# Kernel optimization log

Hardware: AMD Instinct MI355X
Metric: run time of the kernel (lower is better)

## Reference

```python
import jax, jax.numpy as jnp
import numpy as np
import math

HEADS = 8
DIM_HEAD = 64


def setup_inputs() -> dict:
    key = jax.random.key(0)
    k1, k2, k3 = jax.random.split(key, 3)
    b, n, dim = 4, 2048, 512
    inner = HEADS * DIM_HEAD  # 512
    x = jax.random.normal(k1, (b, n, dim), dtype=jnp.float32)
    W_qkv = jax.random.normal(k2, (dim, 4 * inner), dtype=jnp.float32) * (dim ** -0.5)
    W_out = jax.random.normal(k3, (2 * inner, dim), dtype=jnp.float32) * ((2 * inner) ** -0.5)
    b_out = jnp.zeros((dim,), dtype=jnp.float32)
    return {"x": x, "W_qkv": W_qkv, "W_out": W_out, "b_out": b_out}


def reference(x, W_qkv, W_out, b_out):
    b, n, d = x.shape
    h, dh = HEADS, DIM_HEAD
    scale = dh ** -0.5
    qkvt = x @ W_qkv  # [b, n, 4*h*dh]
    q, k, v, t = jnp.split(qkvt, 4, axis=-1)
    # 'b n (h d) -> b h n d'
    def to_heads(z):
        return z.reshape(b, n, h, dh).transpose(0, 2, 1, 3)
    q, k, v, t = map(to_heads, (q, k, v, t))

    # Branch 1: standard softmax attention
    dots = jnp.einsum('bhid,bhjd->bhij', q, k) * scale
    attn1 = jax.nn.softmax(dots, axis=-1)
    out1 = jnp.einsum('bhij,bhjd->bhid', attn1, v)

    # Branch 2: fixed positional-decay attention (shared across b, h; no repeat needed)
    pos = jnp.arange(1, n + 1, dtype=x.dtype)  # linspace(1, n, n)
    tg = jnp.abs(pos[None, :] - pos[:, None])  # |j - i|, [n, n]
    attn2 = jnp.exp(-tg / jnp.asarray(math.e, dtype=x.dtype))
    # NOTE: original divides by sum(-1) WITHOUT keepdim -> broadcasts over columns:
    # attn2[i, j] / sum_k attn2[j, k]
    attn2 = attn2 / attn2.sum(-1)
    out2 = jnp.einsum('ij,bhjd->bhid', attn2, t)

    out = jnp.concatenate([out1, out2], axis=-1)  # [b, h, n, 2*dh]
    out = out.transpose(0, 2, 1, 3).reshape(b, n, 2 * h * dh)  # 'b h n d -> b n (h d)'
    return out @ W_out + b_out
```

## Files before the change

kernel.cpp:

```cpp
#include <hip/hip_runtime.h>
#include <hip/hip_bf16.h>

#define B_ 4
#define N_ 2048
#define D_ 512
#define H_ 8
#define DH_ 64

typedef float float4_ __attribute__((ext_vector_type(4)));
typedef int int2_ __attribute__((ext_vector_type(2)));
typedef int int4_ __attribute__((ext_vector_type(4)));
typedef unsigned short ushort4_ __attribute__((ext_vector_type(4)));
typedef unsigned short ushort8_ __attribute__((ext_vector_type(8)));
typedef __bf16 bf16x8 __attribute__((ext_vector_type(8)));
typedef _Float16 half2_ __attribute__((ext_vector_type(2)));
typedef _Float16 half4_ __attribute__((ext_vector_type(4)));
typedef _Float16 half8_ __attribute__((ext_vector_type(8)));

#if __has_builtin(__builtin_amdgcn_exp2f)
#define EXP2(x) __builtin_amdgcn_exp2f(x)
#else
#define EXP2(x) exp2f(x)
#endif

__device__ __forceinline__ float b2f(unsigned short u) {
  union { unsigned int u; float f; } v; v.u = ((unsigned int)u) << 16; return v.f;
}
__device__ __forceinline__ unsigned short f2b(float f) {
  union { float f; unsigned int u; } v; v.f = f;
  unsigned int r = v.u + 0x7fffu + ((v.u >> 16) & 1u);
  return (unsigned short)(r >> 16);
}
__device__ __forceinline__ half4_ pk4(float a, float b, float c, float d) {
  half2_ lo = __builtin_bit_cast(half2_, __builtin_amdgcn_cvt_pkrtz(a, b));
  half2_ hi = __builtin_bit_cast(half2_, __builtin_amdgcn_cvt_pkrtz(c, d));
  return __builtin_bit_cast(half4_,
      (int2_){__builtin_bit_cast(int, lo), __builtin_bit_cast(int, hi)});
}

#define GLD16(gp, lp)                                                        \
  __builtin_amdgcn_global_load_lds(                                          \
      (const __attribute__((address_space(1))) unsigned int*)(gp),           \
      (__attribute__((address_space(3))) unsigned int*)(lp), 16, 0, 0)

__device__ __forceinline__ bool detect_fp32_local(
    const unsigned short* __restrict__ xhdr, int* cnt_sh) {
  if (threadIdx.x == 0) *cnt_sh = 0;
  __syncthreads();
  unsigned int e = (xhdr[threadIdx.x] >> 7) & 0xFFu;
  if (e >= 134u) atomicAdd(cnt_sh, 1);
  __syncthreads();
  return *cnt_sh > 16;
}

__device__ __forceinline__ void transpose_conv(
    const void* __restrict__ src, unsigned short* __restrict__ dst,
    int R, int C, int bx, int by, bool ofp) {
  __shared__ unsigned short tile[32][33];
  const int c0 = bx * 32, r0 = by * 32;
  const int tx = threadIdx.x & 31, ty = threadIdx.x >> 5;
#pragma unroll
  for (int k = 0; k < 4; ++k) {
    int r = ty + k * 8;
    long idx = (long)(r0 + r) * C + c0 + tx;
    tile[r][tx] = ofp ? f2b(((const float*)src)[idx])
                      : ((const unsigned short*)src)[idx];
  }
  __syncthreads();
#pragma unroll
  for (int k = 0; k < 4; ++k) {
    int c = ty + k * 8;
    dst[(long)(c0 + c) * R + r0 + tx] = tile[tx][c];
  }
}

__global__ __launch_bounds__(256) void prep_all(
    const void* __restrict__ xraw, const void* __restrict__ Wqraw,
    const void* __restrict__ Woraw, unsigned short* __restrict__ xb,
    unsigned short* __restrict__ WqT, unsigned short* __restrict__ WoT,
    unsigned short* __restrict__ Wband) {
  __shared__ int cnt_sh;
  const bool ofp = detect_fp32_local((const unsigned short*)xraw, &cnt_sh);
  const int bid = blockIdx.x;
  if (bid < 4096) {
    int i4 = bid * 256 + threadIdx.x;
    ushort4_ o;
    if (ofp) {
      float4_ v = ((const float4_*)xraw)[i4];
      o[0] = f2b(v[0]); o[1] = f2b(v[1]); o[2] = f2b(v[2]); o[3] = f2b(v[3]);
    } else {
      o = ((const ushort4_*)xraw)[i4];
    }
    *(ushort4_*)(xb + (long)i4 * 4) = o;
  } else if (bid < 5120) {
    const int b2 = bid - 4096;
    transpose_conv(Wqraw, WqT, 512, 2048, b2 % 64, b2 / 64, ofp);
  } else if (bid < 5632) {
    const int b2 = bid - 5120;
    transpose_conv(Woraw, WoT, 1024, 512, b2 % 16, b2 / 16, ofp);
  } else {
    constexpr float INV_E = 0.36787944117144233f;
    constexpr float R1 = 0.69220062755534635f;
    constexpr float INV_1MR = 3.2488706f;
    const int i = bid - 5632;
    const int krel = threadIdx.x;
    const int j = (i >> 6) * 64 - 96 + krel;
    float c = 0.f;
    if (j >= 0 && j < N_) {
      float wgt = __expf(-fabsf((float)(i - j)) * INV_E);
      float rj = __expf(-(float)j * INV_E);
      float rnj = __expf(-(float)(N_ - 1 - j) * INV_E);
      float S = 1.f + R1 * (2.f - rj - rnj) * INV_1MR;
      c = wgt / S;
    }
    _Float16 hv = (_Float16)c;
    Wband[i * 256 + krel] = __builtin_bit_cast(unsigned short, hv);
  }
}

#define MFMA16x32(d, a, b) \
  d = __builtin_amdgcn_mfma_f32_16x16x32_bf16(a, b, d, 0, 0, 0)

__global__ __launch_bounds__(512, 2) void gemm256(
    const unsigned short* __restrict__ A, const unsigned short* __restrict__ Bt,
    unsigned short* __restrict__ C, int M, int N, int K) {
  __shared__ unsigned short As[2][16384];
  __shared__ unsigned short Bs[2][16384];
  const int tid = threadIdx.x;
  const int w = tid >> 6, lane = tid & 63, l16 = lane & 15, quad = lane >> 4;
  const int wm = w >> 2, wn = w & 3;
  const long tm = (long)blockIdx.x * 256, tn = (long)blockIdx.y * 256;

  const int srow = tid >> 3;
  const int sch = (tid & 7) ^ (srow & 7);
  const unsigned short* gA = A + (tm + srow) * (long)K + sch * 8;
  const unsigned short* gB = Bt + (tn + srow) * (long)K + sch * 8;

  const int xr8 = l16 & 7;
  const int ch0 = ((0 + quad) ^ xr8) * 8;
  const int ch1 = ((4 + quad) ^ xr8) * 8;
  const int rowA0 = (wm * 128 + l16) * 64;
  const int rowB0 = (wn * 64 + l16) * 64;

  float4_ acc[8][4] = {};

  auto stage = [&](int t, int bufn) __attribute__((always_inline)) {
#pragma unroll
    for (int r = 0; r < 4; ++r)
      GLD16(gA + (long)(r * 64) * K + t * 64, &As[bufn][r * 4096 + w * 512]);
#pragma unroll
    for (int r = 0; r < 4; ++r)
      GLD16(gB + (long)(r * 64) * K + t * 64, &Bs[bufn][r * 4096 + w * 512]);
  };

  stage(0, 0);
  asm volatile("s_waitcnt vmcnt(0)" ::: "memory");
  __builtin_amdgcn_s_barrier();

  const int NT = K >> 6;
  for (int t = 0; t < NT; ++t) {
    const int buf = t & 1;
    const unsigned short* as = As[buf];
    const unsigned short* bs = Bs[buf];
    bf16x8 af[8], bq[4], br[4];
#pragma unroll
    for (int mi = 0; mi < 4; ++mi) {
      af[mi * 2]     = __builtin_bit_cast(bf16x8, *(const int4_*)&as[rowA0 + mi * 1024 + ch0]);
      af[mi * 2 + 1] = __builtin_bit_cast(bf16x8, *(const int4_*)&as[rowA0 + mi * 1024 + ch1]);
    }
#pragma unroll
    for (int ni = 0; ni < 2; ++ni) {
      bq[ni * 2]     = __builtin_bit_cast(bf16x8, *(const int4_*)&bs[rowB0 + ni * 1024 + ch0]);
      bq[ni * 2 + 1] = __builtin_bit_cast(bf16x8, *(const int4_*)&bs[rowB0 + ni * 1024 + ch1]);
    }
    if (t + 1 < NT) stage(t + 1, buf ^ 1);
    __builtin_amdgcn_s_barrier();
    asm volatile("s_waitcnt lgkmcnt(0)" ::: "memory");
    __builtin_amdgcn_sched_barrier(0);
    __builtin_amdgcn_s_setprio(1);
#pragma unroll
    for (int mi = 0; mi < 4; ++mi)
#pragma unroll
      for (int ni = 0; ni < 2; ++ni) {
        MFMA16x32(acc[mi][ni], af[mi * 2], bq[ni * 2]);
        MFMA16x32(acc[mi][ni], af[mi * 2 + 1], bq[ni * 2 + 1]);
      }
    __builtin_amdgcn_s_setprio(0);
    __builtin_amdgcn_s_barrier();
#pragma unroll
    for (int ni = 0; ni < 2; ++ni) {
      br[ni * 2]     = __builtin_bit_cast(bf16x8, *(const int4_*)&bs[rowB0 + (2 + ni) * 1024 + ch0]);
      br[ni * 2 + 1] = __builtin_bit_cast(bf16x8, *(const int4_*)&bs[rowB0 + (2 + ni) * 1024 + ch1]);
    }
    __builtin_amdgcn_s_barrier();
    asm volatile("s_waitcnt lgkmcnt(0)" ::: "memory");
    __builtin_amdgcn_sched_barrier(0);
    __builtin_amdgcn_s_setprio(1);
#pragma unroll
    for (int mi = 0; mi < 4; ++mi)
#pragma unroll
      for (int ni = 0; ni < 2; ++ni) {
        MFMA16x32(acc[mi][2 + ni], af[mi * 2], br[ni * 2]);
        MFMA16x32(acc[mi][2 + ni], af[mi * 2 + 1], br[ni * 2 + 1]);
      }
    __builtin_amdgcn_s_setprio(0);
    __builtin_amdgcn_s_barrier();
#pragma unroll
    for (int mi = 0; mi < 4; ++mi) {
      af[mi * 2]     = __builtin_bit_cast(bf16x8, *(const int4_*)&as[rowA0 + (4 + mi) * 1024 + ch0]);
      af[mi * 2 + 1] = __builtin_bit_cast(bf16x8, *(const int4_*)&as[rowA0 + (4 + mi) * 1024 + ch1]);
    }
    __builtin_amdgcn_s_barrier();
    asm volatile("s_waitcnt lgkmcnt(0)" ::: "memory");
    __builtin_amdgcn_sched_barrier(0);
    __builtin_amdgcn_s_setprio(1);
#pragma unroll
    for (int mi = 0; mi < 4; ++mi)
#pragma unroll
      for (int ni = 0; ni < 2; ++ni) {
        MFMA16x32(acc[4 + mi][2 + ni], af[mi * 2], br[ni * 2]);
        MFMA16x32(acc[4 + mi][2 + ni], af[mi * 2 + 1], br[ni * 2 + 1]);
      }
    __builtin_amdgcn_s_setprio(0);
    __builtin_amdgcn_s_barrier();
#pragma unroll
    for (int ni = 0; ni < 2; ++ni) {
      bq[ni * 2]     = __builtin_bit_cast(bf16x8, *(const int4_*)&bs[rowB0 + ni * 1024 + ch0]);
      bq[ni * 2 + 1] = __builtin_bit_cast(bf16x8, *(const int4_*)&bs[rowB0 + ni * 1024 + ch1]);
    }
    __builtin_amdgcn_s_barrier();
    asm volatile("s_waitcnt lgkmcnt(0)" ::: "memory");
    __builtin_amdgcn_sched_barrier(0);
    __builtin_amdgcn_s_setprio(1);
#pragma unroll
    for (int mi = 0; mi < 4; ++mi)
#pragma unroll
      for (int ni = 0; ni < 2; ++ni) {
        MFMA16x32(acc[4 + mi][ni], af[mi * 2], bq[ni * 2]);
        MFMA16x32(acc[4 + mi][ni], af[mi * 2 + 1], bq[ni * 2 + 1]);
      }
    __builtin_amdgcn_s_setprio(0);
    asm volatile("s_waitcnt vmcnt(0)" ::: "memory");
    __builtin_amdgcn_sched_barrier(0);
    __builtin_amdgcn_s_barrier();
  }
#pragma unroll
  for (int ni = 0; ni < 4; ++ni) {
    long col = tn + wn * 64 + ni * 16 + l16;
#pragma unroll
    for (int mi = 0; mi < 8; ++mi)
#pragma unroll
      for (int r = 0; r < 4; ++r) {
        long row = tm + wm * 128 + mi * 16 + quad * 4 + r;
        C[row * N + col] = f2b(acc[mi][ni][r]);
      }
  }
}

__global__ __launch_bounds__(256) void gemm_n64(
    const unsigned short* __restrict__ A, const unsigned short* __restrict__ Bt,
    void* __restrict__ C, const void* __restrict__ bias_raw,
    int M, int N, int K, const unsigned short* __restrict__ xhdr) {
  __shared__ int cnt_sh;
  const bool ofp = detect_fp32_local(xhdr, &cnt_sh);
  __shared__ unsigned short As[128 * 32];
  __shared__ unsigned short Bs[64 * 32];
  const int tid = threadIdx.x;
  const int w = tid >> 6, lane = tid & 63, l16 = lane & 15, quad = lane >> 4;
  const int wm = (w & 1) * 64, wn = (w >> 1) * 32;
  const long tm = (long)blockIdx.x * 128, tn = (long)blockIdx.y * 64;
  const int srowA = w * 32 + (lane >> 2);
  const int srowB = w * 16 + (lane >> 2);
  const int scol = (lane & 3) * 8;
  float4_ acc[4][2] = {};
  for (int k0 = 0; k0 < K; k0 += 32) {
#pragma unroll
    for (int q = 0; q < 2; ++q)
      GLD16(&A[(tm + srowA + q * 16) * K + k0 + scol], &As[(w * 32 + q * 16) * 32]);
    GLD16(&Bt[(tn + srowB) * K + k0 + scol], &Bs[(w * 16) * 32]);
    __syncthreads();
    bf16x8 af[4], bf[2];
#pragma unroll
    for (int mb = 0; mb < 4; ++mb)
      af[mb] = __builtin_bit_cast(bf16x8,
          *(const int4_*)&As[(wm + mb * 16 + l16) * 32 + quad * 8]);
#pragma unroll
    for (int nb = 0; nb < 2; ++nb)
      bf[nb] = __builtin_bit_cast(bf16x8,
          *(const int4_*)&Bs[(wn + nb * 16 + l16) * 32 + quad * 8]);
#pragma unroll
    for (int mb = 0; mb < 4; ++mb)
#pragma unroll
      for (int nb = 0; nb < 2; ++nb)
        acc[mb][nb] = __builtin_amdgcn_mfma_f32_16x16x32_bf16(
            af[mb], bf[nb], acc[mb][nb], 0, 0, 0);
    __syncthreads();
  }
#pragma unroll
  for (int nb = 0; nb < 2; ++nb) {
    long col = tn + wn + nb * 16 + l16;
    float bv = ofp ? ((const float*)bias_raw)[col]
                   : b2f(((const unsigned short*)bias_raw)[col]);
#pragma unroll
    for (int mb = 0; mb < 4; ++mb)
#pragma unroll
      for (int r = 0; r < 4; ++r) {
        long row = tm + wm + mb * 16 + quad * 4 + r;
        float val = acc[mb][nb][r] + bv;
        if (ofp) ((float*)C)[row * N + col] = val;
        else ((unsigned short*)C)[row * N + col] = f2b(val);
      }
  }
}

#define TSW 266
__global__ __launch_bounds__(256) void mid_all(
    const unsigned short* __restrict__ qkvt, unsigned short* __restrict__ Vt,
    const unsigned short* __restrict__ Wband, unsigned short* __restrict__ catb) {
  __shared__ __align__(16) unsigned short Ts[64 * TSW];
  const int bid = blockIdx.x;
  const int tid = threadIdx.x;
  if (bid < 512) {
    unsigned int* Td = (unsigned int*)Ts;
    const int bh = bid >> 4, b = bh >> 3, h = bh & 7;
    const int j0 = (bid & 15) * 128;
    const int dg = tid & 7;
#pragma unroll
    for (int it = 0; it < 2; ++it) {
      const int jp = (tid >> 3) + 32 * it;
      const long base =
          (long)(b * N_ + j0 + 2 * jp) * 2048 + 1024 + h * 64 + dg * 8;
      ushort8_ r0 = __builtin_bit_cast(ushort8_, *(const int4_*)&qkvt[base]);
      ushort8_ r1 = __builtin_bit_cast(ushort8_, *(const int4_*)&qkvt[base + 2048]);
#pragma unroll
      for (int e = 0; e < 8; ++e) {
        const int d = dg * 8 + e;
        const int S = (d >> 3) | ((d & 1) << 3);
        unsigned short h0 = __builtin_bit_cast(unsigned short, (_Float16)b2f(r0[e]));
        unsigned short h1 = __builtin_bit_cast(unsigned short, (_Float16)b2f(r1[e]));
        Td[d * 68 + (jp ^ (S << 2))] = (unsigned int)h0 | ((unsigned int)h1 << 16);
      }
    }
    __syncthreads();
#pragma unroll
    for (int it = 0; it < 4; ++it) {
      const int d = (tid >> 4) + 16 * it;
      const int ch = tid & 15;
      const int S = (d >> 3) | ((d & 1) << 3);
      int4_ v = *(const int4_*)&Td[d * 68 + ((ch ^ S) << 2)];
      *(int4_*)&Vt[((long)bh * 64 + d) * 2048 + j0 + ch * 8] = v;
    }
    return;
  }
  const int b2 = bid - 512;
  const int qtile = b2 & 31;
  const int bh = b2 >> 5, b = bh >> 3, h = bh & 7;
  const int jlo = qtile * 64 - 96;
  {
    unsigned int* Tsd = (unsigned int*)Ts;
    const int dg = tid & 7;
#pragma unroll
    for (int it = 0; it < 4; ++it) {
      const int kkp = (tid >> 3) + 32 * it;
      const int jA = jlo + 2 * kkp, jB = jA + 1;
      int4_ r0 = {}, r1 = {};
      if (jA >= 0 && jA < N_)
        r0 = *(const int4_*)&qkvt[(long)(b * N_ + jA) * 2048 + 1536 + h * 64 + dg * 8];
      if (jB >= 0 && jB < N_)
        r1 = *(const int4_*)&qkvt[(long)(b * N_ + jB) * 2048 + 1536 + h * 64 + dg * 8];
      ushort8_ u0 = __builtin_bit_cast(ushort8_, r0);
      ushort8_ u1 = __builtin_bit_cast(ushort8_, r1);
#pragma unroll
      for (int e = 0; e < 8; ++e) {
        const int d = dg * 8 + e;
        unsigned short h0 = __builtin_bit_cast(unsigned short, (_Float16)b2f(u0[e]));
        unsigned short h1 = __builtin_bit_cast(unsigned short, (_Float16)b2f(u1[e]));
        Tsd[d * 133 + kkp] = (unsigned int)h0 | ((unsigned int)h1 << 16);
      }
    }
  }
  __syncthreads();
  const int w = tid >> 6, lane = tid & 63, l16 = lane & 15, quad = lane >> 4;
  const int i_row = qtile * 64 + w * 16 + l16;
  const unsigned short* ap = Wband + i_row * 256;
  float4_ acc[4] = {};
#pragma unroll
  for (int kh = 0; kh < 8; ++kh) {
    half8_ af = __builtin_bit_cast(half8_, *(const int4_*)&ap[kh * 32 + quad * 8]);
#pragma unroll
    for (int nb = 0; nb < 4; ++nb) {
      half8_ bf = __builtin_bit_cast(half8_,
          *(const int4_*)&Ts[(nb * 16 + l16) * TSW + kh * 32 + quad * 8]);
      acc[nb] = __builtin_amdgcn_mfma_f32_16x16x32_f16(af, bf, acc[nb], 0, 0, 0);
    }
  }
#pragma unroll
  for (int nb = 0; nb < 4; ++nb)
#pragma unroll
    for (int r = 0; r < 4; ++r) {
      int row = qtile * 64 + w * 16 + quad * 4 + r;
      catb[(long)(b * N_ + row) * 1024 + h * 128 + 64 + nb * 16 + l16] =
          f2b(acc[nb][r]);
    }
}

__global__ __launch_bounds__(256) void flash_kernel(
    const unsigned short* __restrict__ qkvt, const unsigned short* __restrict__ Vt,
    unsigned short* __restrict__ catb) {
  __shared__ unsigned short Ks[2][64 * 64];
  __shared__ unsigned short Vs[2][64 * 64];
  const int bh = blockIdx.y, b = bh >> 3, h = bh & 7;
  const int i0 = blockIdx.x * 128;
  const int tid = threadIdx.x;
  const int w = tid >> 6, lane = tid & 63, l16 = lane & 15, quad = lane >> 4;
  const int srow8 = lane >> 3, sch = lane & 7;
  const int chK = sch ^ srow8;
  bf16x8 qf[2][2];
  {
    constexpr float SCL = 0.125f * 1.44269504088896f;
#pragma unroll
    for (int s2 = 0; s2 < 2; ++s2) {
      const long qrow =
          (long)(b * N_ + i0 + w * 32 + s2 * 16 + l16) * 2048 + h * 64;
#pragma unroll
      for (int kh = 0; kh < 2; ++kh) {
        ushort8_ raw = __builtin_bit_cast(ushort8_,
            *(const int4_*)&qkvt[qrow + kh * 32 + quad * 8]);
        ushort8_ sc;
#pragma unroll
        for (int e = 0; e < 8; ++e) sc[e] = f2b(b2f(raw[e]) * SCL);
        qf[s2][kh] = __builtin_bit_cast(bf16x8, sc);
      }
    }
  }
  const unsigned short* kp[2];
#pragma unroll
  for (int kh = 0; kh < 2; ++kh)
    kp[kh] = &Ks[0][l16 * 64 + (((kh * 4 + quad) ^ (l16 & 7)) * 8)];
  const unsigned short* vp[4];
#pragma unroll
  for (int c = 0; c < 4; ++c)
    vp[c] = &Vs[0][l16 * 64 + (((c * 2 + (quad >> 1)) ^ (l16 & 7)) * 8) +
                   (quad & 1) * 4];
  const unsigned short* kg[2];
  const unsigned short* vg[2];
#pragma unroll
  for (int g = 0; g < 2; ++g) {
    const int row = w * 16 + g * 8 + srow8;
    kg[g] = qkvt + (long)(b * N_ + row) * 2048 + 512 + h * 64 + chK * 8;
    vg[g] = Vt + ((long)bh * 64 + row) * 2048 + chK * 8;
  }
  float4_ O[2][4] = {};
  float4_ O5[2] = {};
  const half4_ ones = {(_Float16)1.f, (_Float16)1.f, (_Float16)1.f, (_Float16)1.f};

  auto stage = [&](int jt_, int buf_) __attribute__((always_inline)) {
    const int j0 = jt_ * 64;
#pragma unroll
    for (int g = 0; g < 2; ++g) {
      GLD16(kg[g] + (long)j0 * 2048,
            (char*)&Ks[0][0] + buf_ * 8192 + (w * 16 + g * 8) * 128);
      GLD16(vg[g] + j0,
            (char*)&Vs[0][0] + buf_ * 8192 + (w * 16 + g * 8) * 128);
    }
  };
  auto phase = [&](int jt_, int buf_) __attribute__((always_inline)) {
    if (jt_ + 1 < 32) stage(jt_ + 1, buf_ ^ 1);
    float4_ s[2][4] = {};
#pragma unroll
    for (int kh = 0; kh < 2; ++kh)
#pragma unroll
      for (int c = 0; c < 4; ++c) {
        bf16x8 kf = __builtin_bit_cast(bf16x8,
            *(const int4_*)(kp[kh] + buf_ * 4096 + c * 1024));
#pragma unroll
        for (int s2 = 0; s2 < 2; ++s2)
          s[s2][c] = __builtin_amdgcn_mfma_f32_16x16x32_bf16(
              kf, qf[s2][kh], s[s2][c], 0, 0, 0);
      }
    half4_ pf[2][4];
#pragma unroll
    for (int s2 = 0; s2 < 2; ++s2)
#pragma unroll
      for (int c = 0; c < 4; ++c)
        pf[s2][c] = pk4(EXP2(s[s2][c][0]), EXP2(s[s2][c][1]),
                        EXP2(s[s2][c][2]), EXP2(s[s2][c][3]));
#pragma unroll
    for (int c = 0; c < 4; ++c) {
#pragma unroll
      for (int dblk = 0; dblk < 4; ++dblk) {
        half4_ vfv = *(const half4_*)(vp[c] + buf_ * 4096 + dblk * 1024);
#pragma unroll
        for (int s2 = 0; s2 < 2; ++s2)
          O[s2][dblk] = __builtin_amdgcn_mfma_f32_16x16x16f16(
              pf[s2][c], vfv, O[s2][dblk], 0, 0, 0);
      }
#pragma unroll
      for (int s2 = 0; s2 < 2; ++s2)
        O5[s2] = __builtin_amdgcn_mfma_f32_16x16x16f16(
            pf[s2][c], ones, O5[s2], 0, 0, 0);
    }
    __syncthreads();
  };

  stage(0, 0);
  __syncthreads();
  for (int jt = 0; jt < 32; jt += 2) {
    phase(jt, 0);
    phase(jt + 1, 1);
  }
#pragma unroll
  for (int s2 = 0; s2 < 2; ++s2) {
    float linv[4];
#pragma unroll
    for (int r = 0; r < 4; ++r) linv[r] = 1.f / O5[s2][r];
#pragma unroll
    for (int dblk = 0; dblk < 4; ++dblk)
#pragma unroll
      for (int r = 0; r < 4; ++r) {
        int row = i0 + w * 32 + s2 * 16 + quad * 4 + r;
        catb[(long)(b * N_ + row) * 1024 + h * 128 + dblk * 16 + l16] =
            f2b(O[s2][dblk][r] * linv[r]);
      }
  }
}

extern "C" void kernel_launch(void* const* d_in, const int* in_sizes, int n_in,
                              void* d_out, int out_size, void* d_ws, size_t ws_size,
                              hipStream_t stream) {
  char* ws = (char*)d_ws;
  unsigned short* qkvt = (unsigned short*)(ws);
  unsigned short* WqT  = (unsigned short*)(ws + (size_t)32 * 1024 * 1024);
  unsigned short* WoT  = (unsigned short*)(ws + (size_t)34 * 1024 * 1024);
  unsigned short* Vt   = (unsigned short*)(ws + (size_t)35 * 1024 * 1024);
  unsigned short* catb = (unsigned short*)(ws + (size_t)43 * 1024 * 1024);
  unsigned short* xb   = (unsigned short*)(ws + (size_t)59 * 1024 * 1024);
  unsigned short* Wband= (unsigned short*)(ws + (size_t)68 * 1024 * 1024);

  prep_all<<<7680, 256, 0, stream>>>(d_in[0], d_in[1], d_in[2],
                                     xb, WqT, WoT, Wband);
  gemm256<<<dim3(8192 / 256, 2048 / 256), 512, 0, stream>>>(
      xb, WqT, qkvt, 8192, 2048, 512);
  mid_all<<<1536, 256, 0, stream>>>(qkvt, Vt, Wband, catb);
  flash_kernel<<<dim3(2048 / 128, 32), 256, 0, stream>>>(qkvt, Vt, catb);
  gemm_n64<<<dim3(8192 / 128, 512 / 64), 256, 0, stream>>>(
      catb, WoT, d_out, d_in[3], 8192, 512, 1024,
      (const unsigned short*)d_in[0]);
}
```

Before: 190.0 us.

## Rewrite output GEMM with double-buffered swizzled LDS tiles; remap flash block order

```diff
diff --git a/kernel.cpp b/kernel.cpp
--- a/kernel.cpp
+++ b/kernel.cpp
@@ -257,55 +257,94 @@
   }
 }
 
-__global__ __launch_bounds__(256) void gemm_n64(
+__global__ __launch_bounds__(512, 2) void gemm_o(
     const unsigned short* __restrict__ A, const unsigned short* __restrict__ Bt,
     void* __restrict__ C, const void* __restrict__ bias_raw,
-    int M, int N, int K, const unsigned short* __restrict__ xhdr) {
+    const unsigned short* __restrict__ xhdr) {
   __shared__ int cnt_sh;
   const bool ofp = detect_fp32_local(xhdr, &cnt_sh);
-  __shared__ unsigned short As[128 * 32];
-  __shared__ unsigned short Bs[64 * 32];
+  __shared__ unsigned short As[2][8192];
+  __shared__ unsigned short Bs[2][8192];
+  constexpr int K = 1024, N = 512;
   const int tid = threadIdx.x;
   const int w = tid >> 6, lane = tid & 63, l16 = lane & 15, quad = lane >> 4;
-  const int wm = (w & 1) * 64, wn = (w >> 1) * 32;
-  const long tm = (long)blockIdx.x * 128, tn = (long)blockIdx.y * 64;
-  const int srowA = w * 32 + (lane >> 2);
-  const int srowB = w * 16 + (lane >> 2);
-  const int scol = (lane & 3) * 8;
+  const int wm = w >> 2, wn = w & 3;
+  const long tm = (long)blockIdx.x * 128, tn = (long)blockIdx.y * 128;
+  const int srow = tid >> 3;
+  const int sch = (tid & 7) ^ (srow & 7);
+  const unsigned short* gA = A + (tm + srow) * (long)K + sch * 8;
+  const unsigned short* gB = Bt + (tn + srow) * (long)K + sch * 8;
+  const int xr8 = l16 & 7;
+  const int ch0 = ((0 + quad) ^ xr8) * 8;
+  const int ch1 = ((4 + quad) ^ xr8) * 8;
+  const int rowA0 = (wm * 64 + l16) * 64;
+  const int rowB0 = (wn * 32 + l16) * 64;
   float4_ acc[4][2] = {};
-  for (int k0 = 0; k0 < K; k0 += 32) {
-#pragma unroll
-    for (int q = 0; q < 2; ++q)
-      GLD16(&A[(tm + srowA + q * 16) * K + k0 + scol], &As[(w * 32 + q * 16) * 32]);
-    GLD16(&Bt[(tn + srowB) * K + k0 + scol], &Bs[(w * 16) * 32]);
-    __syncthreads();
-    bf16x8 af[4], bf[2];
-#pragma unroll
-    for (int mb = 0; mb < 4; ++mb)
-      af[mb] = __builtin_bit_cast(bf16x8,
-          *(const int4_*)&As[(wm + mb * 16 + l16) * 32 + quad * 8]);
-#pragma unroll
-    for (int nb = 0; nb < 2; ++nb)
-      bf[nb] = __builtin_bit_cast(bf16x8,
-          *(const int4_*)&Bs[(wn + nb * 16 + l16) * 32 + quad * 8]);
-#pragma unroll
-    for (int mb = 0; mb < 4; ++mb)
-#pragma unroll
-      for (int nb = 0; nb < 2; ++nb)
-        acc[mb][nb] = __builtin_amdgcn_mfma_f32_16x16x32_bf16(
-            af[mb], bf[nb], acc[mb][nb], 0, 0, 0);
-    __syncthreads();
+
+  auto stage = [&](int t, int bufn) __attribute__((always_inline)) {
+#pragma unroll
+    for (int r = 0; r < 2; ++r)
+      GLD16(gA + (long)(r * 64) * K + t * 64, &As[bufn][r * 4096 + w * 512]);
+#pragma unroll
+    for (int r = 0; r < 2; ++r)
+      GLD16(gB + (long)(r * 64) * K + t * 64, &Bs[bufn][r * 4096 + w * 512]);
+  };
+
+  stage(0, 0);
+  asm volatile("s_waitcnt vmcnt(0)" ::: "memory");
+  __builtin_amdgcn_s_barrier();
+
+  const int NT = K >> 6;
+  for (int t = 0; t < NT; ++t) {
+    const int buf = t & 1;
+    const unsigned short* as = As[buf];
+    const unsigned short* bs = Bs[buf];
+    bf16x8 af[8], bf0[2], bf1[2];
+#pragma unroll
+    for (int mi = 0; mi < 4; ++mi) {
+      af[mi * 2]     = __builtin_bit_cast(bf16x8, *(const int4_*)&as[rowA0 + mi * 1024 + ch0]);
+      af[mi * 2 + 1] = __builtin_bit_cast(bf16x8, *(const int4_*)&as[rowA0 + mi * 1024 + ch1]);
+    }
+    bf0[0] = __builtin_bit_cast(bf16x8, *(const int4_*)&bs[rowB0 + ch0]);
+    bf0[1] = __builtin_bit_cast(bf16x8, *(const int4_*)&bs[rowB0 + ch1]);
+    if (t + 1 < NT) stage(t + 1, buf ^ 1);
+    __builtin_amdgcn_s_barrier();
+    asm volatile("s_waitcnt lgkmcnt(0)" ::: "memory");
+    __builtin_amdgcn_sched_barrier(0);
+    __builtin_amdgcn_s_setprio(1);
+#pragma unroll
+    for (int mi = 0; mi < 4; ++mi) {
+      MFMA16x32(acc[mi][0], af[mi * 2], bf0[0]);
+      MFMA16x32(acc[mi][0], af[mi * 2 + 1], bf0[1]);
+    }
+    __builtin_amdgcn_s_setprio(0);
+    __builtin_amdgcn_s_barrier();
+    bf1[0] = __builtin_bit_cast(bf16x8, *(const int4_*)&bs[rowB0 + 1024 + ch0]);
+    bf1[1] = __builtin_bit_cast(bf16x8, *(const int4_*)&bs[rowB0 + 1024 + ch1]);
+    __builtin_amdgcn_s_barrier();
+    asm volatile("s_waitcnt lgkmcnt(0)" ::: "memory");
+    __builtin_amdgcn_sched_barrier(0);
+    __builtin_amdgcn_s_setprio(1);
+#pragma unroll
+    for (int mi = 0; mi < 4; ++mi) {
+      MFMA16x32(acc[mi][1], af[mi * 2], bf1[0]);
+      MFMA16x32(acc[mi][1], af[mi * 2 + 1], bf1[1]);
+    }
+    __builtin_amdgcn_s_setprio(0);
+    asm volatile("s_waitcnt vmcnt(0)" ::: "memory");
+    __builtin_amdgcn_sched_barrier(0);
+    __builtin_amdgcn_s_barrier();
   }
 #pragma unroll
   for (int nb = 0; nb < 2; ++nb) {
-    long col = tn + wn + nb * 16 + l16;
+    long col = tn + wn * 32 + nb * 16 + l16;
     float bv = ofp ? ((const float*)bias_raw)[col]
                    : b2f(((const unsigned short*)bias_raw)[col]);
 #pragma unroll
     for (int mb = 0; mb < 4; ++mb)
 #pragma unroll
       for (int r = 0; r < 4; ++r) {
-        long row = tm + wm + mb * 16 + quad * 4 + r;
+        long row = tm + wm * 64 + mb * 16 + quad * 4 + r;
         float val = acc[mb][nb][r] + bv;
         if (ofp) ((float*)C)[row * N + col] = val;
         else ((unsigned short*)C)[row * N + col] = f2b(val);
@@ -409,8 +448,11 @@
     unsigned short* __restrict__ catb) {
   __shared__ unsigned short Ks[2][64 * 64];
   __shared__ unsigned short Vs[2][64 * 64];
-  const int bh = blockIdx.y, b = bh >> 3, h = bh & 7;
-  const int i0 = blockIdx.x * 128;
+  const int flat = blockIdx.x + blockIdx.y * 16;
+  const int slot = flat & 7, idx = flat >> 3;
+  const int bh = slot * 4 + (idx >> 4);
+  const int i0 = (idx & 15) * 128;
+  const int b = bh >> 3, h = bh & 7;
   const int tid = threadIdx.x;
   const int w = tid >> 6, lane = tid & 63, l16 = lane & 15, quad = lane >> 4;
   const int srow8 = lane >> 3, sch = lane & 7;
@@ -543,7 +585,6 @@
       xb, WqT, qkvt, 8192, 2048, 512);
   mid_all<<<1536, 256, 0, stream>>>(qkvt, Vt, Wband, catb);
   flash_kernel<<<dim3(2048 / 128, 32), 256, 0, stream>>>(qkvt, Vt, catb);
-  gemm_n64<<<dim3(8192 / 128, 512 / 64), 256, 0, stream>>>(
-      catb, WoT, d_out, d_in[3], 8192, 512, 1024,
-      (const unsigned short*)d_in[0]);
-}
+  gemm_o<<<dim3(8192 / 128, 512 / 128), 512, 0, stream>>>(
+      catb, WoT, d_out, d_in[3], (const unsigned short*)d_in[0]);
+}
```

Result: no change. 186.3 us (-1.9%).
